# Kernel tuning notes

Hardware: AMD Instinct MI355X
Metric: run time of the kernel (lower is better)

Reference implementation:

```python
import jax, jax.numpy as jnp
import numpy as np

T, IN, H, NL = 512, 1024, 2048, 2  # seq_len, input dim, hidden, num_layers


def _lstm_cell(x, h, c, Wih, Whh, bih, bhh):
    # PyTorch gate order: i, f, g, o
    g = x @ Wih.T + h @ Whh.T + bih + bhh  # [B, 4H]
    i, f, gg, o = jnp.split(g, 4, axis=-1)
    c_new = jax.nn.sigmoid(f) * c + jax.nn.sigmoid(i) * jnp.tanh(gg)
    h_new = jax.nn.sigmoid(o) * jnp.tanh(c_new)
    return h_new, c_new


def setup_inputs() -> dict:
    key = jax.random.key(0)
    ks = jax.random.split(key, 24)
    s = 0.02

    def w(k, shape):
        return (jax.random.normal(k, shape, jnp.float32) * s)

    z4h = jnp.zeros((4 * H,), jnp.float32)
    return {
        "features": jax.random.normal(ks[0], (T, 1, IN), jnp.float32),
        "epsilon": jax.random.normal(ks[1], (NL, H), jnp.float32),
        # encoder LSTM layer 0 / layer 1
        "Wih0_e": w(ks[2], (4 * H, IN)), "Whh0_e": w(ks[3], (4 * H, H)),
        "bih0_e": z4h, "bhh0_e": z4h,
        "Wih1_e": w(ks[4], (4 * H, H)), "Whh1_e": w(ks[5], (4 * H, H)),
        "bih1_e": z4h, "bhh1_e": z4h,
        # mu / var heads
        "Wmu": w(ks[6], (H, H)), "bmu": jnp.zeros((H,), jnp.float32),
        "Wvar": w(ks[7], (H, H)), "bvar": jnp.zeros((H,), jnp.float32),
        # decoder stacked cells layer 0 / layer 1
        "Wih0_d": w(ks[8], (4 * H, H)), "Whh0_d": w(ks[9], (4 * H, H)),
        "bih0_d": z4h, "bhh0_d": z4h,
        "Wih1_d": w(ks[10], (4 * H, H)), "Whh1_d": w(ks[11], (4 * H, H)),
        "bih1_d": z4h, "bhh1_d": z4h,
        # output projection 2048 -> 1024
        "Wout": w(ks[12], (IN, H)), "bout": jnp.zeros((IN,), jnp.float32),
    }


def reference(features, epsilon,
              Wih0_e, Whh0_e, bih0_e, bhh0_e,
              Wih1_e, Whh1_e, bih1_e, bhh1_e,
              Wmu, bmu, Wvar, bvar,
              Wih0_d, Whh0_d, bih0_d, bhh0_d,
              Wih1_d, Whh1_d, bih1_d, bhh1_d,
              Wout, bout):
    seq_len = features.shape[0]
    B = features.shape[1]  # 1
    z1 = jnp.zeros((B, H), features.dtype)

    # ---- encoder: 2-layer LSTM over time, keep final (h, c) per layer ----
    def enc_step(carry, x_t):
        h0, c0, h1, c1 = carry
        h0, c0 = _lstm_cell(x_t, h0, c0, Wih0_e, Whh0_e, bih0_e, bhh0_e)
        h1, c1 = _lstm_cell(h0, h1, c1, Wih1_e, Whh1_e, bih1_e, bhh1_e)
        return (h0, c0, h1, c1), None

    (h0, c0, h1, c1), _ = jax.lax.scan(enc_step, (z1, z1, z1, z1), features)
    h_last = jnp.stack([h0, h1])  # [2, 1, H]
    c_last = jnp.stack([c0, c1])  # [2, 1, H]

    # ---- variational heads + reparameterize ----
    hs = h_last.squeeze(1)                       # [2, H]
    h_mu = hs @ Wmu.T + bmu                      # [2, H]
    h_log_variance = jnp.log(jax.nn.softplus(hs @ Wvar.T + bvar))
    std = jnp.exp(0.5 * h_log_variance)
    z = (h_mu + epsilon * std)[:, None, :]       # [2, 1, H]

    # ---- decoder: unrolled stacked LSTM cells, zero first input ----
    def dec_step(carry, _):
        x, dh0, dc0, dh1, dc1 = carry
        dh0, dc0 = _lstm_cell(x, dh0, dc0, Wih0_d, Whh0_d, bih0_d, bhh0_d)
        dh1, dc1 = _lstm_cell(dh0, dh1, dc1, Wih1_d, Whh1_d, bih1_d, bhh1_d)
        out_t = dh1 @ Wout.T + bout              # [1, 1024]
        return (dh1, dh0, dc0, dh1, dc1), out_t

    init = (z1, z[0], c_last[0], z[1], c_last[1])
    _, outs = jax.lax.scan(dec_step, init, None, length=seq_len)
    decoded_features = outs[::-1]                # reversed, [seq_len, 1, 1024]

    return h_mu, h_log_variance, decoded_features
```

## Files before the change

### kernel.cpp

```cpp
#include <hip/hip_runtime.h>

#define NB 512
#define NT 256
#define HD 2048
#define IND 1024
#define TS 512

#define SL_GENF 0
#define SL_GENA 1
#define SL_GENB 2
#define SL_FLF  3
#define SL_FLA  (3 + 512)
#define SL_FLB  (3 + 512 + 256)
#define N_SLOTS (3 + 512 + 256 + 256)

struct Params {
  const float* features;
  const float* eps;
  const float* fW[11];
  const void*  W[11];
  const float* bih0e; const float* bhh0e;
  const float* bih1e; const float* bhh1e;
  const float* bmu;   const float* bvar;
  const float* bih0d; const float* bhh0d;
  const float* bih1d; const float* bhh1d;
  const float* bout;
  float* out;
  float* act;
  unsigned* ctrl;
};

__device__ __constant__ size_t kWSizes[11] = {
  8388608ull,16777216ull,16777216ull,16777216ull,4194304ull,4194304ull,
  16777216ull,16777216ull,16777216ull,16777216ull,2097152ull };

__device__ __forceinline__ float4 w4(const unsigned short* w) {
  uint2 v = *(const uint2*)w;
  float4 r;
  r.x = __uint_as_float(v.x << 16);
  r.y = __uint_as_float(v.x & 0xFFFF0000u);
  r.z = __uint_as_float(v.y << 16);
  r.w = __uint_as_float(v.y & 0xFFFF0000u);
  return r;
}
__device__ __forceinline__ float4 w4(const float* w) { return *(const float4*)w; }

__device__ __forceinline__ unsigned pk(float lo, float hi) {
  unsigned a = __float_as_uint(lo), b = __float_as_uint(hi);
  a = (a + 0x7FFFu + ((a >> 16) & 1u)) >> 16;
  b = (b + 0x7FFFu + ((b >> 16) & 1u)) >> 16;
  return a | (b << 16);
}

__device__ __forceinline__ float wred(float v) {
  v += __shfl_xor(v, 1);  v += __shfl_xor(v, 2);  v += __shfl_xor(v, 4);
  v += __shfl_xor(v, 8);  v += __shfl_xor(v, 16); v += __shfl_xor(v, 32);
  return v;
}

__device__ __forceinline__ float sigm(float x) { return 1.f / (1.f + __expf(-x)); }

__device__ __forceinline__ unsigned ld_rlx(unsigned* p) {
  return __hip_atomic_load(p, __ATOMIC_RELAXED, __HIP_MEMORY_SCOPE_AGENT);
}
__device__ __forceinline__ unsigned ld_acq(unsigned* p) {
  return __hip_atomic_load(p, __ATOMIC_ACQUIRE, __HIP_MEMORY_SCOPE_AGENT);
}
__device__ __forceinline__ void st_rel(unsigned* p, unsigned v) {
  __hip_atomic_store(p, v, __ATOMIC_RELEASE, __HIP_MEMORY_SCOPE_AGENT);
}

__device__ __forceinline__ void barrier_sync(unsigned* ctrl, int flags_slot0, int n,
                                             int myidx, bool leader, int gen_slot,
                                             unsigned target) {
  __syncthreads();
  if (threadIdx.x == 0) st_rel(ctrl + (size_t)(flags_slot0 + myidx) * 16, target);
  if (leader) {
    bool done = false;
    while (!done) {
      bool mine = true;
      for (int i = threadIdx.x; i < n; i += NT)
        mine = mine && (ld_rlx(ctrl + (size_t)(flags_slot0 + i) * 16) >= target);
      done = (bool)__syncthreads_and((int)mine);
      if (!done && threadIdx.x == 0) __builtin_amdgcn_s_sleep(1);
    }
    if (threadIdx.x == 0) {
      (void)ld_acq(ctrl + (size_t)flags_slot0 * 16);
      st_rel(ctrl + (size_t)gen_slot * 16, target);
    }
  } else {
    if (threadIdx.x == 0) {
      while (ld_rlx(ctrl + (size_t)gen_slot * 16) < target) __builtin_amdgcn_s_sleep(2);
      (void)ld_acq(ctrl + (size_t)gen_slot * 16);
    }
  }
  __syncthreads();
}

__device__ __forceinline__ void wait_gen(unsigned* ctrl, int gen_slot, unsigned target) {
  if (threadIdx.x == 0) {
    while (ld_rlx(ctrl + (size_t)gen_slot * 16) < target) __builtin_amdgcn_s_sleep(2);
    (void)ld_acq(ctrl + (size_t)gen_slot * 16);
  }
  __syncthreads();
}

template<typename WT, int U>
__device__ __forceinline__ void dotU(const WT* __restrict__ W, int K,
                                     const float* __restrict__ xs, int lane, float* acc) {
  for (int k = lane * 4; k < K; k += 256) {
    float4 xv = *(const float4*)(xs + k);
#pragma unroll
    for (int r = 0; r < U; ++r) {
      float4 wv = w4(W + (size_t)r * K + k);
      acc[r] = fmaf(wv.x, xv.x, fmaf(wv.y, xv.y, fmaf(wv.z, xv.z, fmaf(wv.w, xv.w, acc[r]))));
    }
  }
}

template<typename WT, int U>
__device__ void cell_phase(const WT* __restrict__ Wih, const WT* __restrict__ Whh,
                           const float* __restrict__ bih, const float* __restrict__ bhh,
                           const float* __restrict__ xg, int Kx,
                           const float* __restrict__ hg,
                           float* __restrict__ hout, float* __restrict__ cbuf, int j0,
                           const WT* __restrict__ Wo, const float* __restrict__ bo,
                           float* __restrict__ odst, int orow0,
                           float* lds) {
  const int tid = threadIdx.x;
  float* xs  = lds;
  float* hs  = lds + Kx;
  float* gld = lds + Kx + HD;
  for (int i = tid * 4; i < Kx; i += NT * 4) *(float4*)(xs + i) = *(const float4*)(xg + i);
  for (int i = tid * 4; i < HD; i += NT * 4) *(float4*)(hs + i) = *(const float4*)(hg + i);
  __syncthreads();
  const int wave = tid >> 6, lane = tid & 63;
  const size_t row0 = (size_t)wave * HD + j0;
  float acc[U];
#pragma unroll
  for (int r = 0; r < U; ++r) acc[r] = 0.f;
  dotU<WT, U>(Wih + row0 * (size_t)Kx, Kx, xs, lane, acc);
  dotU<WT, U>(Whh + row0 * (size_t)HD, HD, hs, lane, acc);
#pragma unroll
  for (int r = 0; r < U; ++r) {
    float s = wred(acc[r]);
    if (lane == 0) gld[wave * U + r] = s;
  }
  if (Wo != nullptr && wave < 2) {
    const int row = orow0 + wave;
    const WT* wr = Wo + (size_t)row * HD;
    float a = 0.f;
    for (int k = lane * 4; k < HD; k += 256) {
      float4 wv = w4(wr + k);
      float4 xv = *(const float4*)(xs + k);
      a = fmaf(wv.x, xv.x, fmaf(wv.y, xv.y, fmaf(wv.z, xv.z, fmaf(wv.w, xv.w, a))));
    }
    a = wred(a);
    if (lane == 0) odst[row] = a + bo[row];
  }
  __syncthreads();
  if (tid < U) {
    const int j = j0 + tid;
    float gi = gld[0 * U + tid] + bih[j]          + bhh[j];
    float gf = gld[1 * U + tid] + bih[HD + j]     + bhh[HD + j];
    float gc = gld[2 * U + tid] + bih[2 * HD + j] + bhh[2 * HD + j];
    float go = gld[3 * U + tid] + bih[3 * HD + j] + bhh[3 * HD + j];
    float c  = cbuf[j];
    float cn = sigm(gf) * c + sigm(gi) * tanhf(gc);
    float hn = sigm(go) * tanhf(cn);
    cbuf[j] = cn;
    hout[j] = hn;
  }
}

__global__ void init_kernel(unsigned* ctrl, float* act) {
  const int t = threadIdx.x;
  for (int i = t; i < N_SLOTS * 16; i += 256) ctrl[i] = 0u;
  for (int i = t; i < 30720; i += 256) act[i] = 0.f;
}

template<typename WT>
__global__ __launch_bounds__(NT, 2) void vae_kernel(Params p) {
  __shared__ float lds[2 * HD + 64];
  const int tid = threadIdx.x;
  unsigned* ctrl = p.ctrl;
  float* act = p.act;
  float* h0b = act;
  float* c0  = act + 4096;
  float* h1b = act + 6144;
  float* c1  = act + 10240;
  float* dh0 = act + 12288;
  float* dh1 = act + 16384;
  float* mu  = act + 20480;
  float* sp  = act + 24576;
  float* zb  = act + 28672;

  unsigned gf = 0;

  if constexpr (sizeof(WT) == 2) {
    const size_t gsz = (size_t)gridDim.x * NT;
    const size_t g0  = (size_t)blockIdx.x * NT + tid;
    for (int m = 0; m < 11; ++m) {
      if (m == 4 || m == 5) continue;
      const float* s = p.fW[m];
      unsigned short* d = (unsigned short*)p.W[m];
      const size_t n = kWSizes[m];
      for (size_t i = g0 * 8; i < n; i += gsz * 8) {
        float4 a = *(const float4*)(s + i);
        float4 b = *(const float4*)(s + i + 4);
        uint4 o;
        o.x = pk(a.x, a.y); o.y = pk(a.z, a.w);
        o.z = pk(b.x, b.y); o.w = pk(b.z, b.w);
        *(uint4*)(d + i) = o;
      }
    }
  }
  ++gf;
  barrier_sync(ctrl, SL_FLF, NB, blockIdx.x, blockIdx.x == 0, SL_GENF, gf);

  const WT* Wih0e = (const WT*)p.W[0];
  const WT* Whh0e = (const WT*)p.W[1];
  const WT* Wih1e = (const WT*)p.W[2];
  const WT* Whh1e = (const WT*)p.W[3];
  const WT* Wih0d = (const WT*)p.W[6];
  const WT* Whh0d = (const WT*)p.W[7];
  const WT* Wih1d = (const WT*)p.W[8];
  const WT* Whh1d = (const WT*)p.W[9];
  const WT* Wout  = (const WT*)p.W[10];

  if (blockIdx.x < 256) {
    const int bb = blockIdx.x;
    for (int t = 0; t < TS; ++t) {
      if (t >= 2) wait_gen(ctrl, SL_GENB, (unsigned)(t - 1));
      cell_phase<WT, 8>(Wih0e, Whh0e, p.bih0e, p.bhh0e,
                        p.features + (size_t)t * IND, IND,
                        h0b + (t & 1) * HD, h0b + ((t + 1) & 1) * HD, c0, bb * 8,
                        (const WT*)nullptr, nullptr, nullptr, 0, lds);
      barrier_sync(ctrl, SL_FLA, 256, bb, bb == 0, SL_GENA, (unsigned)(t + 1));
    }
  } else {
    const int bb = blockIdx.x - 256;
    for (int t = 0; t < TS; ++t) {
      wait_gen(ctrl, SL_GENA, (unsigned)(t + 1));
      cell_phase<WT, 8>(Wih1e, Whh1e, p.bih1e, p.bhh1e,
                        h0b + ((t + 1) & 1) * HD, HD,
                        h1b + (t & 1) * HD, h1b + ((t + 1) & 1) * HD, c1, bb * 8,
                        (const WT*)nullptr, nullptr, nullptr, 0, lds);
      barrier_sync(ctrl, SL_FLB, 256, bb, bb == 0, SL_GENB, (unsigned)(t + 1));
    }
  }
  ++gf;
  barrier_sync(ctrl, SL_FLF, NB, blockIdx.x, blockIdx.x == 0, SL_GENF, gf);

  {
    const int b = blockIdx.x;
    const bool isVar = b >= 256;
    const int u0 = (isVar ? b - 256 : b) * 16;
    const int s  = u0 >> 11;
    const int i0 = u0 & 2047;
    const float* hsrc = s ? h1b : h0b;
    float* xs = lds;
    for (int i = tid * 4; i < HD; i += NT * 4) *(float4*)(xs + i) = *(const float4*)(hsrc + i);
    __syncthreads();
    const float* Wl = isVar ? p.fW[5] : p.fW[4];
    const int wave = tid >> 6, lane = tid & 63;
    const int ri = i0 + wave * 4;
    float acc[4] = {0.f, 0.f, 0.f, 0.f};
    dotU<float, 4>(Wl + (size_t)ri * HD, HD, xs, lane, acc);
#pragma unroll
    for (int r = 0; r < 4; ++r) {
      float v = wred(acc[r]);
      if (lane == 0) {
        const int i = ri + r;
        if (!isVar) {
          float m = v + p.bmu[i];
          p.out[s * HD + i] = m;
          mu[s * HD + i] = m;
        } else {
          float vv = v + p.bvar[i];
          float spv = (vv > 15.f) ? vv : log1pf(__expf(vv));
          p.out[4096 + s * HD + i] = __logf(spv);
          sp[s * HD + i] = spv;
        }
      }
    }
  }
  ++gf;
  barrier_sync(ctrl, SL_FLF, NB, blockIdx.x, blockIdx.x == 0, SL_GENF, gf);

  if (blockIdx.x < 16) {
    const int idx = blockIdx.x * NT + tid;
    const float z = mu[idx] + p.eps[idx] * sqrtf(sp[idx]);
    if (idx < HD) dh0[idx] = z;
    else          dh1[idx - HD] = z;
  }
  ++gf;
  barrier_sync(ctrl, SL_FLF, NB, blockIdx.x, blockIdx.x == 0, SL_GENF, gf);

  for (int t = 0; t < TS; ++t) {
    const float* xdec = t ? (dh1 + (t & 1) * HD) : zb;
    cell_phase<WT, 4>(Wih0d, Whh0d, p.bih0d, p.bhh0d,
                      xdec, HD,
                      dh0 + (t & 1) * HD, dh0 + ((t + 1) & 1) * HD, c0, blockIdx.x * 4,
                      t ? Wout : (const WT*)nullptr, p.bout,
                      p.out + 8192 + (size_t)(512 - t) * IND, blockIdx.x * 2, lds);
    ++gf;
    barrier_sync(ctrl, SL_FLF, NB, blockIdx.x, blockIdx.x == 0, SL_GENF, gf);
    cell_phase<WT, 4>(Wih1d, Whh1d, p.bih1d, p.bhh1d,
                      dh0 + ((t + 1) & 1) * HD, HD,
                      dh1 + (t & 1) * HD, dh1 + ((t + 1) & 1) * HD, c1, blockIdx.x * 4,
                      (const WT*)nullptr, nullptr, nullptr, 0, lds);
    ++gf;
    barrier_sync(ctrl, SL_FLF, NB, blockIdx.x, blockIdx.x == 0, SL_GENF, gf);
  }

  {
    float* xs = lds;
    const float* xg = dh1;
    for (int i = tid * 4; i < HD; i += NT * 4) *(float4*)(xs + i) = *(const float4*)(xg + i);
    __syncthreads();
    const int wave = tid >> 6, lane = tid & 63;
    if (wave < 2) {
      const int row = blockIdx.x * 2 + wave;
      const WT* wr = Wout + (size_t)row * HD;
      float a = 0.f;
      for (int k = lane * 4; k < HD; k += 256) {
        float4 wv = w4(wr + k);
        float4 xv = *(const float4*)(xs + k);
        a = fmaf(wv.x, xv.x, fmaf(wv.y, xv.y, fmaf(wv.z, xv.z, fmaf(wv.w, xv.w, a))));
      }
      a = wred(a);
      if (lane == 0) p.out[8192 + row] = a + p.bout[row];
    }
  }
}

extern "C" void kernel_launch(void* const* d_in, const int* in_sizes, int n_in,
                              void* d_out, int out_size, void* d_ws, size_t ws_size,
                              hipStream_t stream) {
  (void)in_sizes; (void)n_in; (void)out_size;
  Params p;
  p.features = (const float*)d_in[0];
  p.eps      = (const float*)d_in[1];
  const int wIdx[11] = {2, 3, 6, 7, 10, 12, 14, 15, 18, 19, 22};
  static const size_t wsizes[11] = {
    8388608ull,16777216ull,16777216ull,16777216ull,4194304ull,4194304ull,
    16777216ull,16777216ull,16777216ull,16777216ull,2097152ull };
  for (int m = 0; m < 11; ++m) p.fW[m] = (const float*)d_in[wIdx[m]];
  p.bih0e = (const float*)d_in[4];  p.bhh0e = (const float*)d_in[5];
  p.bih1e = (const float*)d_in[8];  p.bhh1e = (const float*)d_in[9];
  p.bmu   = (const float*)d_in[11]; p.bvar  = (const float*)d_in[13];
  p.bih0d = (const float*)d_in[16]; p.bhh0d = (const float*)d_in[17];
  p.bih1d = (const float*)d_in[20]; p.bhh1d = (const float*)d_in[21];
  p.bout  = (const float*)d_in[23];
  p.out = (float*)d_out;

  char* ws = (char*)d_ws;
  p.ctrl = (unsigned*)ws;
  const size_t ctrl_bytes = (size_t)N_SLOTS * 64;
  const size_t act_off = (ctrl_bytes + 255) & ~(size_t)255;
  p.act = (float*)(ws + act_off);
  const size_t base = act_off + ((30720 * 4 + 255) & ~(size_t)255);
  size_t total = 0;
  for (int m = 0; m < 11; ++m) total += wsizes[m];
  const bool bf = ws_size >= base + total * 2;
  if (bf) {
    char* wp = ws + base;
    for (int m = 0; m < 11; ++m) { p.W[m] = wp; wp += wsizes[m] * 2; }
  } else {
    for (int m = 0; m < 11; ++m) p.W[m] = p.fW[m];
  }

  init_kernel<<<dim3(1), dim3(256), 0, stream>>>(p.ctrl, p.act);
  void* args[] = { &p };
  if (bf) {
    hipLaunchCooperativeKernel(reinterpret_cast<void*>(vae_kernel<unsigned short>),
                               dim3(NB), dim3(NT), args, 0, stream);
  } else {
    hipLaunchCooperativeKernel(reinterpret_cast<void*>(vae_kernel<float>),
                               dim3(NB), dim3(NT), args, 0, stream);
  }
}
```

Measured before the change: 44.17 ms.

## Keep LSTM weights resident in registers and LDS as bf16 across timesteps

Replaces the streaming-weight design with a persistent kernel where each wave owns one hidden unit and loads that unit's four gate rows once, packed to bf16, into registers plus shared memory. The weights are reused for all 512 timesteps, so the per-step global weight traffic goes away. The grid moves to 256 blocks of 512 threads, the leader-based barrier becomes an all-blocks polling barrier, and the cell state stays in registers. The cost is very high register pressure (192 packed words per thread) and large LDS use, which risks spills or failed cooperative launch. Encoder layers now run serialized rather than pipelined across block halves.

New measurement: 71.90 ms. 62.8% more time.

```diff
diff --git a/kernel.cpp b/kernel.cpp
--- a/kernel.cpp
+++ b/kernel.cpp
@@ -1,24 +1,20 @@
 #include <hip/hip_runtime.h>
 
-#define NB 512
-#define NT 256
+
+#define NB 256
+#define NT 512
 #define HD 2048
-#define IND 1024
 #define TS 512
-
-#define SL_GENF 0
-#define SL_GENA 1
-#define SL_GENB 2
-#define SL_FLF  3
-#define SL_FLA  (3 + 512)
-#define SL_FLB  (3 + 512 + 256)
-#define N_SLOTS (3 + 512 + 256 + 256)
 
 struct Params {
   const float* features;
   const float* eps;
-  const float* fW[11];
-  const void*  W[11];
+  const float* Wih0e; const float* Whh0e;
+  const float* Wih1e; const float* Whh1e;
+  const float* Wmu;   const float* Wvar;
+  const float* Wih0d; const float* Whh0d;
+  const float* Wih1d; const float* Whh1d;
+  const float* Wout;
   const float* bih0e; const float* bhh0e;
   const float* bih1e; const float* bhh1e;
   const float* bmu;   const float* bvar;
@@ -30,34 +26,23 @@
   unsigned* ctrl;
 };
 
-__device__ __constant__ size_t kWSizes[11] = {
-  8388608ull,16777216ull,16777216ull,16777216ull,4194304ull,4194304ull,
-  16777216ull,16777216ull,16777216ull,16777216ull,2097152ull };
-
-__device__ __forceinline__ float4 w4(const unsigned short* w) {
-  uint2 v = *(const uint2*)w;
-  float4 r;
-  r.x = __uint_as_float(v.x << 16);
-  r.y = __uint_as_float(v.x & 0xFFFF0000u);
-  r.z = __uint_as_float(v.y << 16);
-  r.w = __uint_as_float(v.y & 0xFFFF0000u);
-  return r;
-}
-__device__ __forceinline__ float4 w4(const float* w) { return *(const float4*)w; }
-
 __device__ __forceinline__ unsigned pk(float lo, float hi) {
   unsigned a = __float_as_uint(lo), b = __float_as_uint(hi);
   a = (a + 0x7FFFu + ((a >> 16) & 1u)) >> 16;
   b = (b + 0x7FFFu + ((b >> 16) & 1u)) >> 16;
   return a | (b << 16);
 }
-
+__device__ __forceinline__ float2 up(unsigned u) {
+  float2 r;
+  r.x = __uint_as_float(u << 16);
+  r.y = __uint_as_float(u & 0xFFFF0000u);
+  return r;
+}
 __device__ __forceinline__ float wred(float v) {
   v += __shfl_xor(v, 1);  v += __shfl_xor(v, 2);  v += __shfl_xor(v, 4);
   v += __shfl_xor(v, 8);  v += __shfl_xor(v, 16); v += __shfl_xor(v, 32);
   return v;
 }
-
 __device__ __forceinline__ float sigm(float x) { return 1.f / (1.f + __expf(-x)); }
 
 __device__ __forceinline__ unsigned ld_rlx(unsigned* p) {
@@ -70,314 +55,319 @@
   __hip_atomic_store(p, v, __ATOMIC_RELEASE, __HIP_MEMORY_SCOPE_AGENT);
 }
 
-__device__ __forceinline__ void barrier_sync(unsigned* ctrl, int flags_slot0, int n,
-                                             int myidx, bool leader, int gen_slot,
-                                             unsigned target) {
+__device__ __forceinline__ void gbar(unsigned* ctrl, unsigned target) {
   __syncthreads();
-  if (threadIdx.x == 0) st_rel(ctrl + (size_t)(flags_slot0 + myidx) * 16, target);
-  if (leader) {
-    bool done = false;
-    while (!done) {
-      bool mine = true;
-      for (int i = threadIdx.x; i < n; i += NT)
-        mine = mine && (ld_rlx(ctrl + (size_t)(flags_slot0 + i) * 16) >= target);
-      done = (bool)__syncthreads_and((int)mine);
-      if (!done && threadIdx.x == 0) __builtin_amdgcn_s_sleep(1);
-    }
-    if (threadIdx.x == 0) {
-      (void)ld_acq(ctrl + (size_t)flags_slot0 * 16);
-      st_rel(ctrl + (size_t)gen_slot * 16, target);
-    }
-  } else {
-    if (threadIdx.x == 0) {
-      while (ld_rlx(ctrl + (size_t)gen_slot * 16) < target) __builtin_amdgcn_s_sleep(2);
-      (void)ld_acq(ctrl + (size_t)gen_slot * 16);
-    }
-  }
+  if (threadIdx.x == 0) st_rel(ctrl + (size_t)(1 + blockIdx.x) * 16, target);
+  bool done = false;
+  while (!done) {
+    bool mine = true;
+    if (threadIdx.x < NB)
+      mine = (ld_rlx(ctrl + (size_t)(1 + threadIdx.x) * 16) >= target);
+    done = (bool)__syncthreads_and((int)mine);
+  }
+  if (threadIdx.x == 0) (void)ld_acq(ctrl);
   __syncthreads();
 }
 
-__device__ __forceinline__ void wait_gen(unsigned* ctrl, int gen_slot, unsigned target) {
-  if (threadIdx.x == 0) {
-    while (ld_rlx(ctrl + (size_t)gen_slot * 16) < target) __builtin_amdgcn_s_sleep(2);
-    (void)ld_acq(ctrl + (size_t)gen_slot * 16);
-  }
-  __syncthreads();
-}
-
-template<typename WT, int U>
-__device__ __forceinline__ void dotU(const WT* __restrict__ W, int K,
-                                     const float* __restrict__ xs, int lane, float* acc) {
-  for (int k = lane * 4; k < K; k += 256) {
-    float4 xv = *(const float4*)(xs + k);
-#pragma unroll
-    for (int r = 0; r < U; ++r) {
-      float4 wv = w4(W + (size_t)r * K + k);
-      acc[r] = fmaf(wv.x, xv.x, fmaf(wv.y, xv.y, fmaf(wv.z, xv.z, fmaf(wv.w, xv.w, acc[r]))));
-    }
-  }
-}
-
-template<typename WT, int U>
-__device__ void cell_phase(const WT* __restrict__ Wih, const WT* __restrict__ Whh,
-                           const float* __restrict__ bih, const float* __restrict__ bhh,
-                           const float* __restrict__ xg, int Kx,
-                           const float* __restrict__ hg,
-                           float* __restrict__ hout, float* __restrict__ cbuf, int j0,
-                           const WT* __restrict__ Wo, const float* __restrict__ bo,
-                           float* __restrict__ odst, int orow0,
-                           float* lds) {
+template<int RR0, int CV, int CL, int O, int M>
+__device__ __forceinline__ void loadmat(unsigned (&wv)[8][24], unsigned (*lw)[NT],
+                                        const float* __restrict__ W, int K,
+                                        int u, int lane, int tid) {
+#pragma unroll
+  for (int q = 0; q < 4; ++q) {
+    const float* rp = W + (size_t)(q * HD + u) * K + 4 * lane;
+#pragma unroll
+    for (int cb = 0; cb < CV; ++cb) {
+      float4 f = *(const float4*)(rp + cb * 256);
+      wv[RR0 + q][O + 2 * cb]     = pk(f.x, f.y);
+      wv[RR0 + q][O + 2 * cb + 1] = pk(f.z, f.w);
+    }
+#pragma unroll
+    for (int j = 0; j < CL; ++j) {
+      float4 f = *(const float4*)(rp + (CV + j) * 256);
+      lw[(RR0 + q) * 8 + M * 4 + 2 * j][tid]     = pk(f.x, f.y);
+      lw[(RR0 + q) * 8 + M * 4 + 2 * j + 1][tid] = pk(f.z, f.w);
+    }
+  }
+}
+
+template<int RR0, int XV, int XL, int XO, int HO>
+__device__ __forceinline__ void cell4(const unsigned (&wv)[8][24],
+                                      const unsigned (*lw)[NT],
+                                      const float* __restrict__ xs,
+                                      const float* __restrict__ hs,
+                                      int lane, int tid, float* g) {
+  float a0 = 0.f, a1 = 0.f, a2 = 0.f, a3 = 0.f;
+#pragma unroll
+  for (int cb = 0; cb < XV + XL; ++cb) {
+    float4 xv = *(const float4*)(xs + cb * 256 + 4 * lane);
+    unsigned u0, u1, u2, u3, u4, u5, u6, u7;
+    if (cb < XV) {
+      u0 = wv[RR0 + 0][XO + 2 * cb]; u1 = wv[RR0 + 0][XO + 2 * cb + 1];
+      u2 = wv[RR0 + 1][XO + 2 * cb]; u3 = wv[RR0 + 1][XO + 2 * cb + 1];
+      u4 = wv[RR0 + 2][XO + 2 * cb]; u5 = wv[RR0 + 2][XO + 2 * cb + 1];
+      u6 = wv[RR0 + 3][XO + 2 * cb]; u7 = wv[RR0 + 3][XO + 2 * cb + 1];
+    } else {
+      const int j = cb - XV;
+      u0 = lw[(RR0 + 0) * 8 + 2 * j][tid]; u1 = lw[(RR0 + 0) * 8 + 2 * j + 1][tid];
+      u2 = lw[(RR0 + 1) * 8 + 2 * j][tid]; u3 = lw[(RR0 + 1) * 8 + 2 * j + 1][tid];
+      u4 = lw[(RR0 + 2) * 8 + 2 * j][tid]; u5 = lw[(RR0 + 2) * 8 + 2 * j + 1][tid];
+      u6 = lw[(RR0 + 3) * 8 + 2 * j][tid]; u7 = lw[(RR0 + 3) * 8 + 2 * j + 1][tid];
+    }
+    float2 p0 = up(u0), p1 = up(u1), p2 = up(u2), p3 = up(u3);
+    float2 p4 = up(u4), p5 = up(u5), p6 = up(u6), p7 = up(u7);
+    a0 = fmaf(p0.x, xv.x, a0); a0 = fmaf(p0.y, xv.y, a0);
+    a0 = fmaf(p1.x, xv.z, a0); a0 = fmaf(p1.y, xv.w, a0);
+    a1 = fmaf(p2.x, xv.x, a1); a1 = fmaf(p2.y, xv.y, a1);
+    a1 = fmaf(p3.x, xv.z, a1); a1 = fmaf(p3.y, xv.w, a1);
+    a2 = fmaf(p4.x, xv.x, a2); a2 = fmaf(p4.y, xv.y, a2);
+    a2 = fmaf(p5.x, xv.z, a2); a2 = fmaf(p5.y, xv.w, a2);
+    a3 = fmaf(p6.x, xv.x, a3); a3 = fmaf(p6.y, xv.y, a3);
+    a3 = fmaf(p7.x, xv.z, a3); a3 = fmaf(p7.y, xv.w, a3);
+  }
+#pragma unroll
+  for (int cb = 0; cb < 8; ++cb) {
+    float4 hv = *(const float4*)(hs + cb * 256 + 4 * lane);
+    unsigned u0, u1, u2, u3, u4, u5, u6, u7;
+    if (cb < 6) {
+      u0 = wv[RR0 + 0][HO + 2 * cb]; u1 = wv[RR0 + 0][HO + 2 * cb + 1];
+      u2 = wv[RR0 + 1][HO + 2 * cb]; u3 = wv[RR0 + 1][HO + 2 * cb + 1];
+      u4 = wv[RR0 + 2][HO + 2 * cb]; u5 = wv[RR0 + 2][HO + 2 * cb + 1];
+      u6 = wv[RR0 + 3][HO + 2 * cb]; u7 = wv[RR0 + 3][HO + 2 * cb + 1];
+    } else {
+      const int j = cb - 6;
+      u0 = lw[(RR0 + 0) * 8 + 4 + 2 * j][tid]; u1 = lw[(RR0 + 0) * 8 + 4 + 2 * j + 1][tid];
+      u2 = lw[(RR0 + 1) * 8 + 4 + 2 * j][tid]; u3 = lw[(RR0 + 1) * 8 + 4 + 2 * j + 1][tid];
+      u4 = lw[(RR0 + 2) * 8 + 4 + 2 * j][tid]; u5 = lw[(RR0 + 2) * 8 + 4 + 2 * j + 1][tid];
+      u6 = lw[(RR0 + 3) * 8 + 4 + 2 * j][tid]; u7 = lw[(RR0 + 3) * 8 + 4 + 2 * j + 1][tid];
+    }
+    float2 p0 = up(u0), p1 = up(u1), p2 = up(u2), p3 = up(u3);
+    float2 p4 = up(u4), p5 = up(u5), p6 = up(u6), p7 = up(u7);
+    a0 = fmaf(p0.x, hv.x, a0); a0 = fmaf(p0.y, hv.y, a0);
+    a0 = fmaf(p1.x, hv.z, a0); a0 = fmaf(p1.y, hv.w, a0);
+    a1 = fmaf(p2.x, hv.x, a1); a1 = fmaf(p2.y, hv.y, a1);
+    a1 = fmaf(p3.x, hv.z, a1); a1 = fmaf(p3.y, hv.w, a1);
+    a2 = fmaf(p4.x, hv.x, a2); a2 = fmaf(p4.y, hv.y, a2);
+    a2 = fmaf(p5.x, hv.z, a2); a2 = fmaf(p5.y, hv.w, a2);
+    a3 = fmaf(p6.x, hv.x, a3); a3 = fmaf(p6.y, hv.y, a3);
+    a3 = fmaf(p7.x, hv.z, a3); a3 = fmaf(p7.y, hv.w, a3);
+  }
+  g[0] = wred(a0); g[1] = wred(a1); g[2] = wred(a2); g[3] = wred(a3);
+}
+
+__device__ __forceinline__ void fuse(const float* g, const float* __restrict__ bih,
+                                     const float* __restrict__ bhh, int u,
+                                     float& c, float* hdst, int lane) {
+  float gi = g[0] + bih[u]        + bhh[u];
+  float gf = g[1] + bih[2048 + u] + bhh[2048 + u];
+  float gc = g[2] + bih[4096 + u] + bhh[4096 + u];
+  float go = g[3] + bih[6144 + u] + bhh[6144 + u];
+  float cn = sigm(gf) * c + sigm(gi) * tanhf(gc);
+  c = cn;
+  if (lane == 0) hdst[u] = sigm(go) * tanhf(cn);
+}
+
+__global__ void init_kernel(unsigned* ctrl) {
+  for (int i = threadIdx.x; i < (1 + NB) * 16; i += 256) ctrl[i] = 0u;
+}
+
+__global__ __launch_bounds__(NT, 2) void vae_kernel(Params p) {
+  __shared__ unsigned lw[64][NT];
+  __shared__ float st[2 * HD];
+  float* stx = st;
+  float* sth = st + HD;
+
   const int tid = threadIdx.x;
-  float* xs  = lds;
-  float* hs  = lds + Kx;
-  float* gld = lds + Kx + HD;
-  for (int i = tid * 4; i < Kx; i += NT * 4) *(float4*)(xs + i) = *(const float4*)(xg + i);
-  for (int i = tid * 4; i < HD; i += NT * 4) *(float4*)(hs + i) = *(const float4*)(hg + i);
-  __syncthreads();
   const int wave = tid >> 6, lane = tid & 63;
-  const size_t row0 = (size_t)wave * HD + j0;
-  float acc[U];
-#pragma unroll
-  for (int r = 0; r < U; ++r) acc[r] = 0.f;
-  dotU<WT, U>(Wih + row0 * (size_t)Kx, Kx, xs, lane, acc);
-  dotU<WT, U>(Whh + row0 * (size_t)HD, HD, hs, lane, acc);
-#pragma unroll
-  for (int r = 0; r < U; ++r) {
-    float s = wred(acc[r]);
-    if (lane == 0) gld[wave * U + r] = s;
-  }
-  if (Wo != nullptr && wave < 2) {
-    const int row = orow0 + wave;
-    const WT* wr = Wo + (size_t)row * HD;
-    float a = 0.f;
-    for (int k = lane * 4; k < HD; k += 256) {
-      float4 wv = w4(wr + k);
-      float4 xv = *(const float4*)(xs + k);
-      a = fmaf(wv.x, xv.x, fmaf(wv.y, xv.y, fmaf(wv.z, xv.z, fmaf(wv.w, xv.w, a))));
-    }
-    a = wred(a);
-    if (lane == 0) odst[row] = a + bo[row];
-  }
-  __syncthreads();
-  if (tid < U) {
-    const int j = j0 + tid;
-    float gi = gld[0 * U + tid] + bih[j]          + bhh[j];
-    float gf = gld[1 * U + tid] + bih[HD + j]     + bhh[HD + j];
-    float gc = gld[2 * U + tid] + bih[2 * HD + j] + bhh[2 * HD + j];
-    float go = gld[3 * U + tid] + bih[3 * HD + j] + bhh[3 * HD + j];
-    float c  = cbuf[j];
-    float cn = sigm(gf) * c + sigm(gi) * tanhf(gc);
-    float hn = sigm(go) * tanhf(cn);
-    cbuf[j] = cn;
-    hout[j] = hn;
-  }
-}
-
-__global__ void init_kernel(unsigned* ctrl, float* act) {
-  const int t = threadIdx.x;
-  for (int i = t; i < N_SLOTS * 16; i += 256) ctrl[i] = 0u;
-  for (int i = t; i < 30720; i += 256) act[i] = 0.f;
-}
-
-template<typename WT>
-__global__ __launch_bounds__(NT, 2) void vae_kernel(Params p) {
-  __shared__ float lds[2 * HD + 64];
-  const int tid = threadIdx.x;
+  const int b = blockIdx.x;
+  const int u = b * 8 + wave;
   unsigned* ctrl = p.ctrl;
   float* act = p.act;
-  float* h0b = act;
-  float* c0  = act + 4096;
-  float* h1b = act + 6144;
-  float* c1  = act + 10240;
-  float* dh0 = act + 12288;
-  float* dh1 = act + 16384;
-  float* mu  = act + 20480;
-  float* sp  = act + 24576;
-  float* zb  = act + 28672;
-
+  float* h0b  = act;
+  float* h1b  = act + 4096;
+  float* dh0b = act + 8192;
+  float* dh1b = act + 12288;
+  float* mub  = act + 16384;
+  float* spb  = act + 20480;
   unsigned gf = 0;
-
-  if constexpr (sizeof(WT) == 2) {
-    const size_t gsz = (size_t)gridDim.x * NT;
-    const size_t g0  = (size_t)blockIdx.x * NT + tid;
-    for (int m = 0; m < 11; ++m) {
-      if (m == 4 || m == 5) continue;
-      const float* s = p.fW[m];
-      unsigned short* d = (unsigned short*)p.W[m];
-      const size_t n = kWSizes[m];
-      for (size_t i = g0 * 8; i < n; i += gsz * 8) {
-        float4 a = *(const float4*)(s + i);
-        float4 b = *(const float4*)(s + i + 4);
-        uint4 o;
-        o.x = pk(a.x, a.y); o.y = pk(a.z, a.w);
-        o.z = pk(b.x, b.y); o.w = pk(b.z, b.w);
-        *(uint4*)(d + i) = o;
-      }
-    }
-  }
-  ++gf;
-  barrier_sync(ctrl, SL_FLF, NB, blockIdx.x, blockIdx.x == 0, SL_GENF, gf);
-
-  const WT* Wih0e = (const WT*)p.W[0];
-  const WT* Whh0e = (const WT*)p.W[1];
-  const WT* Wih1e = (const WT*)p.W[2];
-  const WT* Whh1e = (const WT*)p.W[3];
-  const WT* Wih0d = (const WT*)p.W[6];
-  const WT* Whh0d = (const WT*)p.W[7];
-  const WT* Wih1d = (const WT*)p.W[8];
-  const WT* Whh1d = (const WT*)p.W[9];
-  const WT* Wout  = (const WT*)p.W[10];
-
-  if (blockIdx.x < 256) {
-    const int bb = blockIdx.x;
-    for (int t = 0; t < TS; ++t) {
-      if (t >= 2) wait_gen(ctrl, SL_GENB, (unsigned)(t - 1));
-      cell_phase<WT, 8>(Wih0e, Whh0e, p.bih0e, p.bhh0e,
-                        p.features + (size_t)t * IND, IND,
-                        h0b + (t & 1) * HD, h0b + ((t + 1) & 1) * HD, c0, bb * 8,
-                        (const WT*)nullptr, nullptr, nullptr, 0, lds);
-      barrier_sync(ctrl, SL_FLA, 256, bb, bb == 0, SL_GENA, (unsigned)(t + 1));
-    }
-  } else {
-    const int bb = blockIdx.x - 256;
-    for (int t = 0; t < TS; ++t) {
-      wait_gen(ctrl, SL_GENA, (unsigned)(t + 1));
-      cell_phase<WT, 8>(Wih1e, Whh1e, p.bih1e, p.bhh1e,
-                        h0b + ((t + 1) & 1) * HD, HD,
-                        h1b + (t & 1) * HD, h1b + ((t + 1) & 1) * HD, c1, bb * 8,
-                        (const WT*)nullptr, nullptr, nullptr, 0, lds);
-      barrier_sync(ctrl, SL_FLB, 256, bb, bb == 0, SL_GENB, (unsigned)(t + 1));
-    }
-  }
-  ++gf;
-  barrier_sync(ctrl, SL_FLF, NB, blockIdx.x, blockIdx.x == 0, SL_GENF, gf);
+  float g[4];
+
+  unsigned wv[8][24];
+  float c0 = 0.f, c1 = 0.f;
+
+  loadmat<0, 4, 0, 0, 0>(wv, lw, p.Wih0e, 1024, u, lane, tid);
+  loadmat<0, 6, 2, 8, 1>(wv, lw, p.Whh0e, 2048, u, lane, tid);
+  loadmat<4, 6, 2, 0, 0>(wv, lw, p.Wih1e, 2048, u, lane, tid);
+  loadmat<4, 6, 2, 12, 1>(wv, lw, p.Whh1e, 2048, u, lane, tid);
+
+  for (int t = 0; t < TS; ++t) {
+    if (tid < 256)
+      *(float4*)(stx + tid * 4) = *(const float4*)(p.features + (size_t)t * 1024 + tid * 4);
+    if (t == 0) {
+      float4 z; z.x = 0.f; z.y = 0.f; z.z = 0.f; z.w = 0.f;
+      *(float4*)(sth + tid * 4) = z;
+    } else {
+      *(float4*)(sth + tid * 4) = *(const float4*)(h0b + (t & 1) * HD + tid * 4);
+    }
+    __syncthreads();
+    cell4<0, 4, 0, 0, 8>(wv, lw, stx, sth, lane, tid, g);
+    fuse(g, p.bih0e, p.bhh0e, u, c0, h0b + ((t + 1) & 1) * HD, lane);
+    gbar(ctrl, ++gf);
+
+    *(float4*)(stx + tid * 4) = *(const float4*)(h0b + ((t + 1) & 1) * HD + tid * 4);
+    if (t == 0) {
+      float4 z; z.x = 0.f; z.y = 0.f; z.z = 0.f; z.w = 0.f;
+      *(float4*)(sth + tid * 4) = z;
+    } else {
+      *(float4*)(sth + tid * 4) = *(const float4*)(h1b + (t & 1) * HD + tid * 4);
+    }
+    __syncthreads();
+    cell4<4, 6, 2, 0, 12>(wv, lw, stx, sth, lane, tid, g);
+    fuse(g, p.bih1e, p.bhh1e, u, c1, h1b + ((t + 1) & 1) * HD, lane);
+    gbar(ctrl, ++gf);
+  }
 
   {
-    const int b = blockIdx.x;
-    const bool isVar = b >= 256;
-    const int u0 = (isVar ? b - 256 : b) * 16;
-    const int s  = u0 >> 11;
-    const int i0 = u0 & 2047;
-    const float* hsrc = s ? h1b : h0b;
-    float* xs = lds;
-    for (int i = tid * 4; i < HD; i += NT * 4) *(float4*)(xs + i) = *(const float4*)(hsrc + i);
-    __syncthreads();
-    const float* Wl = isVar ? p.fW[5] : p.fW[4];
-    const int wave = tid >> 6, lane = tid & 63;
-    const int ri = i0 + wave * 4;
-    float acc[4] = {0.f, 0.f, 0.f, 0.f};
-    dotU<float, 4>(Wl + (size_t)ri * HD, HD, xs, lane, acc);
-#pragma unroll
-    for (int r = 0; r < 4; ++r) {
-      float v = wred(acc[r]);
-      if (lane == 0) {
-        const int i = ri + r;
+    *(float4*)(stx + tid * 4) = *(const float4*)(h0b + tid * 4);
+    *(float4*)(sth + tid * 4) = *(const float4*)(h1b + tid * 4);
+    __syncthreads();
+    const bool isVar = (b >= 128);
+    const int r0 = (b & 127) * 16 + wave * 2;
+    const float* Wl = isVar ? p.Wvar : p.Wmu;
+    const float* rp0 = Wl + (size_t)r0 * HD + 4 * lane;
+    const float* rp1 = rp0 + HD;
+    float a00 = 0.f, a01 = 0.f, a10 = 0.f, a11 = 0.f;
+#pragma unroll
+    for (int cb = 0; cb < 8; ++cb) {
+      float4 w0 = *(const float4*)(rp0 + cb * 256);
+      float4 w1 = *(const float4*)(rp1 + cb * 256);
+      float4 xv = *(const float4*)(stx + cb * 256 + 4 * lane);
+      float4 hv = *(const float4*)(sth + cb * 256 + 4 * lane);
+      a00 = fmaf(w0.x, xv.x, fmaf(w0.y, xv.y, fmaf(w0.z, xv.z, fmaf(w0.w, xv.w, a00))));
+      a01 = fmaf(w0.x, hv.x, fmaf(w0.y, hv.y, fmaf(w0.z, hv.z, fmaf(w0.w, hv.w, a01))));
+      a10 = fmaf(w1.x, xv.x, fmaf(w1.y, xv.y, fmaf(w1.z, xv.z, fmaf(w1.w, xv.w, a10))));
+      a11 = fmaf(w1.x, hv.x, fmaf(w1.y, hv.y, fmaf(w1.z, hv.z, fmaf(w1.w, hv.w, a11))));
+    }
+    a00 = wred(a00); a01 = wred(a01); a10 = wred(a10); a11 = wred(a11);
+    if (lane == 0) {
+#pragma unroll
+      for (int r = 0; r < 2; ++r) {
+        const int i = r0 + r;
+        const float vx = r ? a10 : a00;
+        const float vh = r ? a11 : a01;
         if (!isVar) {
-          float m = v + p.bmu[i];
-          p.out[s * HD + i] = m;
-          mu[s * HD + i] = m;
+          float m0 = vx + p.bmu[i], m1 = vh + p.bmu[i];
+          p.out[i] = m0;        mub[i] = m0;
+          p.out[HD + i] = m1;   mub[HD + i] = m1;
         } else {
-          float vv = v + p.bvar[i];
-          float spv = (vv > 15.f) ? vv : log1pf(__expf(vv));
-          p.out[4096 + s * HD + i] = __logf(spv);
-          sp[s * HD + i] = spv;
+          float v0 = vx + p.bvar[i], v1 = vh + p.bvar[i];
+          float s0 = (v0 > 15.f) ? v0 : log1pf(__expf(v0));
+          float s1 = (v1 > 15.f) ? v1 : log1pf(__expf(v1));
+          p.out[4096 + i] = __logf(s0);      spb[i] = s0;
+          p.out[4096 + HD + i] = __logf(s1); spb[HD + i] = s1;
         }
       }
     }
   }
-  ++gf;
-  barrier_sync(ctrl, SL_FLF, NB, blockIdx.x, blockIdx.x == 0, SL_GENF, gf);
-
-  if (blockIdx.x < 16) {
-    const int idx = blockIdx.x * NT + tid;
-    const float z = mu[idx] + p.eps[idx] * sqrtf(sp[idx]);
-    if (idx < HD) dh0[idx] = z;
-    else          dh1[idx - HD] = z;
-  }
-  ++gf;
-  barrier_sync(ctrl, SL_FLF, NB, blockIdx.x, blockIdx.x == 0, SL_GENF, gf);
+  gbar(ctrl, ++gf);
+
+  loadmat<0, 6, 2, 0, 0>(wv, lw, p.Wih0d, 2048, u, lane, tid);
+  loadmat<0, 6, 2, 12, 1>(wv, lw, p.Whh0d, 2048, u, lane, tid);
+  loadmat<4, 6, 2, 0, 0>(wv, lw, p.Wih1d, 2048, u, lane, tid);
+  loadmat<4, 6, 2, 12, 1>(wv, lw, p.Whh1d, 2048, u, lane, tid);
 
   for (int t = 0; t < TS; ++t) {
-    const float* xdec = t ? (dh1 + (t & 1) * HD) : zb;
-    cell_phase<WT, 4>(Wih0d, Whh0d, p.bih0d, p.bhh0d,
-                      xdec, HD,
-                      dh0 + (t & 1) * HD, dh0 + ((t + 1) & 1) * HD, c0, blockIdx.x * 4,
-                      t ? Wout : (const WT*)nullptr, p.bout,
-                      p.out + 8192 + (size_t)(512 - t) * IND, blockIdx.x * 2, lds);
-    ++gf;
-    barrier_sync(ctrl, SL_FLF, NB, blockIdx.x, blockIdx.x == 0, SL_GENF, gf);
-    cell_phase<WT, 4>(Wih1d, Whh1d, p.bih1d, p.bhh1d,
-                      dh0 + ((t + 1) & 1) * HD, HD,
-                      dh1 + (t & 1) * HD, dh1 + ((t + 1) & 1) * HD, c1, blockIdx.x * 4,
-                      (const WT*)nullptr, nullptr, nullptr, 0, lds);
-    ++gf;
-    barrier_sync(ctrl, SL_FLF, NB, blockIdx.x, blockIdx.x == 0, SL_GENF, gf);
-  }
-
-  {
-    float* xs = lds;
-    const float* xg = dh1;
-    for (int i = tid * 4; i < HD; i += NT * 4) *(float4*)(xs + i) = *(const float4*)(xg + i);
-    __syncthreads();
-    const int wave = tid >> 6, lane = tid & 63;
-    if (wave < 2) {
-      const int row = blockIdx.x * 2 + wave;
-      const WT* wr = Wout + (size_t)row * HD;
+    if (t == 0) {
+      float4 z; z.x = 0.f; z.y = 0.f; z.z = 0.f; z.w = 0.f;
+      *(float4*)(stx + tid * 4) = z;
+      float4 m = *(const float4*)(mub + tid * 4);
+      float4 e = *(const float4*)(p.eps + tid * 4);
+      float4 s = *(const float4*)(spb + tid * 4);
+      float4 zv;
+      zv.x = m.x + e.x * sqrtf(s.x); zv.y = m.y + e.y * sqrtf(s.y);
+      zv.z = m.z + e.z * sqrtf(s.z); zv.w = m.w + e.w * sqrtf(s.w);
+      *(float4*)(sth + tid * 4) = zv;
+    } else {
+      *(float4*)(stx + tid * 4) = *(const float4*)(dh1b + (t & 1) * HD + tid * 4);
+      *(float4*)(sth + tid * 4) = *(const float4*)(dh0b + (t & 1) * HD + tid * 4);
+    }
+    __syncthreads();
+    cell4<0, 6, 2, 0, 12>(wv, lw, stx, sth, lane, tid, g);
+    fuse(g, p.bih0d, p.bhh0d, u, c0, dh0b + ((t + 1) & 1) * HD, lane);
+    if (t > 0 && wave < 4) {
+      const int orow = b * 4 + wave;
+      const float* wr = p.Wout + (size_t)orow * HD + 4 * lane;
       float a = 0.f;
-      for (int k = lane * 4; k < HD; k += 256) {
-        float4 wv = w4(wr + k);
-        float4 xv = *(const float4*)(xs + k);
-        a = fmaf(wv.x, xv.x, fmaf(wv.y, xv.y, fmaf(wv.z, xv.z, fmaf(wv.w, xv.w, a))));
+#pragma unroll
+      for (int cb = 0; cb < 8; ++cb) {
+        float4 w4v = *(const float4*)(wr + cb * 256);
+        float4 xv = *(const float4*)(stx + cb * 256 + 4 * lane);
+        a = fmaf(w4v.x, xv.x, fmaf(w4v.y, xv.y, fmaf(w4v.z, xv.z, fmaf(w4v.w, xv.w, a))));
       }
       a = wred(a);
-      if (lane == 0) p.out[8192 + row] = a + p.bout[row];
-    }
+      if (lane == 0) p.out[8192 + (size_t)(512 - t) * 1024 + orow] = a + p.bout[orow];
+    }
+    gbar(ctrl, ++gf);
+
+    *(float4*)(sth + tid * 4) = *(const float4*)(dh0b + ((t + 1) & 1) * HD + tid * 4);
+    if (t == 0) {
+      float4 m = *(const float4*)(mub + HD + tid * 4);
+      float4 e = *(const float4*)(p.eps + HD + tid * 4);
+      float4 s = *(const float4*)(spb + HD + tid * 4);
+      float4 zv;
+      zv.x = m.x + e.x * sqrtf(s.x); zv.y = m.y + e.y * sqrtf(s.y);
+      zv.z = m.z + e.z * sqrtf(s.z); zv.w = m.w + e.w * sqrtf(s.w);
+      *(float4*)(stx + tid * 4) = zv;
+    }
+    __syncthreads();
+    cell4<4, 6, 2, 0, 12>(wv, lw, sth, stx, lane, tid, g);
+    fuse(g, p.bih1d, p.bhh1d, u, c1, dh1b + ((t + 1) & 1) * HD, lane);
+    gbar(ctrl, ++gf);
+  }
+
+  *(float4*)(stx + tid * 4) = *(const float4*)(dh1b + tid * 4);
+  __syncthreads();
+  if (wave < 4) {
+    const int orow = b * 4 + wave;
+    const float* wr = p.Wout + (size_t)orow * HD + 4 * lane;
+    float a = 0.f;
+#pragma unroll
+    for (int cb = 0; cb < 8; ++cb) {
+      float4 w4v = *(const float4*)(wr + cb * 256);
+      float4 xv = *(const float4*)(stx + cb * 256 + 4 * lane);
+      a = fmaf(w4v.x, xv.x, fmaf(w4v.y, xv.y, fmaf(w4v.z, xv.z, fmaf(w4v.w, xv.w, a))));
+    }
+    a = wred(a);
+    if (lane == 0) p.out[8192 + orow] = a + p.bout[orow];
   }
 }
 
 extern "C" void kernel_launch(void* const* d_in, const int* in_sizes, int n_in,
                               void* d_out, int out_size, void* d_ws, size_t ws_size,
                               hipStream_t stream) {
-  (void)in_sizes; (void)n_in; (void)out_size;
+  (void)in_sizes; (void)n_in; (void)out_size; (void)ws_size;
   Params p;
   p.features = (const float*)d_in[0];
   p.eps      = (const float*)d_in[1];
-  const int wIdx[11] = {2, 3, 6, 7, 10, 12, 14, 15, 18, 19, 22};
-  static const size_t wsizes[11] = {
-    8388608ull,16777216ull,16777216ull,16777216ull,4194304ull,4194304ull,
-    16777216ull,16777216ull,16777216ull,16777216ull,2097152ull };
-  for (int m = 0; m < 11; ++m) p.fW[m] = (const float*)d_in[wIdx[m]];
+  p.Wih0e = (const float*)d_in[2];  p.Whh0e = (const float*)d_in[3];
   p.bih0e = (const float*)d_in[4];  p.bhh0e = (const float*)d_in[5];
+  p.Wih1e = (const float*)d_in[6];  p.Whh1e = (const float*)d_in[7];
   p.bih1e = (const float*)d_in[8];  p.bhh1e = (const float*)d_in[9];
-  p.bmu   = (const float*)d_in[11]; p.bvar  = (const float*)d_in[13];
+  p.Wmu   = (const float*)d_in[10]; p.bmu   = (const float*)d_in[11];
+  p.Wvar  = (const float*)d_in[12]; p.bvar  = (const float*)d_in[13];
+  p.Wih0d = (const float*)d_in[14]; p.Whh0d = (const float*)d_in[15];
   p.bih0d = (const float*)d_in[16]; p.bhh0d = (const float*)d_in[17];
+  p.Wih1d = (const float*)d_in[18]; p.Whh1d = (const float*)d_in[19];
   p.bih1d = (const float*)d_in[20]; p.bhh1d = (const float*)d_in[21];
-  p.bout  = (const float*)d_in[23];
+  p.Wout  = (const float*)d_in[22]; p.bout  = (const float*)d_in[23];
   p.out = (float*)d_out;
 
   char* ws = (char*)d_ws;
   p.ctrl = (unsigned*)ws;
-  const size_t ctrl_bytes = (size_t)N_SLOTS * 64;
-  const size_t act_off = (ctrl_bytes + 255) & ~(size_t)255;
-  p.act = (float*)(ws + act_off);
-  const size_t base = act_off + ((30720 * 4 + 255) & ~(size_t)255);
-  size_t total = 0;
-  for (int m = 0; m < 11; ++m) total += wsizes[m];
-  const bool bf = ws_size >= base + total * 2;
-  if (bf) {
-    char* wp = ws + base;
-    for (int m = 0; m < 11; ++m) { p.W[m] = wp; wp += wsizes[m] * 2; }
-  } else {
-    for (int m = 0; m < 11; ++m) p.W[m] = p.fW[m];
-  }
-
-  init_kernel<<<dim3(1), dim3(256), 0, stream>>>(p.ctrl, p.act);
+  p.act  = (float*)(ws + 32768);
+
+  init_kernel<<<dim3(1), dim3(256), 0, stream>>>(p.ctrl);
   void* args[] = { &p };
-  if (bf) {
-    hipLaunchCooperativeKernel(reinterpret_cast<void*>(vae_kernel<unsigned short>),
-                               dim3(NB), dim3(NT), args, 0, stream);
-  } else {
-    hipLaunchCooperativeKernel(reinterpret_cast<void*>(vae_kernel<float>),
-                               dim3(NB), dim3(NT), args, 0, stream);
-  }
-}
+  hipLaunchCooperativeKernel(reinterpret_cast<void*>(vae_kernel),
+                             dim3(NB), dim3(NT), args, 0, stream);
+}
```
